# Performance work log

Measured on AMD Instinct MI355X. Metric: run time of the kernel, lower is better.

Reference implementation:

```python
import jax, jax.numpy as jnp
import numpy as np

N = 1_000_000
D_MODEL = 128
D_PRIN = 64        # d_principle: truncated projected dims used in traversal stage
R = 32             # nsw32 -> fixed out-degree
B = 128            # query batch
E = 32             # random32 entry points
EF = 64            # ef_search (beam width)
K = 10
N_ITERS = 8        # fixed number of beam-expansion rounds (jit-friendly traversal)


def setup_inputs() -> dict:
    key = jax.random.key(0)
    k1, k2, k3, k4, k5 = jax.random.split(key, 5)
    query = jax.random.normal(k1, (B, D_MODEL), jnp.float32)
    VT = jax.random.normal(k2, (D_MODEL, D_MODEL), jnp.float32) / jnp.sqrt(D_MODEL)
    storage = jax.random.normal(k3, (N, D_MODEL), jnp.float32)
    neighbors = jax.random.randint(k4, (N, R), 0, N, jnp.int32)
    entry_ids = jax.random.randint(k5, (E,), 0, N, jnp.int32)
    return {"query": query, "VT": VT, "storage": storage,
            "neighbors": neighbors, "entry_ids": entry_ids,
            "k": K, "ef_search": EF}


def _search(query, VT, storage, neighbors, entry_ids, k, ef_search):
    n = storage.shape[0]
    bq = query.shape[0]
    BIG = jnp.float32(1e30)

    # stage 0: project query into SVD basis; principle dims for traversal
    q_full = query @ VT.T                      # [B, d_model]
    q_p = q_full[:, :D_PRIN]                   # [B, d_p]
    storage_p = storage[:, :D_PRIN]            # [N, d_p]
    sq_p = jnp.sum(storage_p * storage_p, axis=-1)          # [N]
    qn = jnp.sum(q_p * q_p, axis=-1, keepdims=True)         # [B, 1]

    def dist_p(ids):  # squared L2 in principle dims, sentinel id >= n -> BIG
        c = jnp.clip(ids, 0, n - 1)
        d = sq_p[c] - 2.0 * jnp.einsum('bmd,bd->bm', storage_p[c], q_p) + qn
        return jnp.where(ids >= n, BIG, d)

    def dedup_topk(ids, dists, m):
        # sort by id, mask duplicate ids (same id -> same dist), keep best m
        order = jnp.argsort(ids, axis=-1)
        sid = jnp.take_along_axis(ids, order, axis=-1)
        sd = jnp.take_along_axis(dists, order, axis=-1)
        dup = jnp.concatenate(
            [jnp.zeros_like(sid[:, :1], dtype=bool), sid[:, 1:] == sid[:, :-1]], axis=-1)
        sd = jnp.where(dup | (sid >= n), BIG, sd)
        neg, idx = jax.lax.top_k(-sd, m)
        return jnp.take_along_axis(sid, idx, axis=-1), -neg

    # entry stage (random32): distances to fixed entry points
    ids0 = jnp.broadcast_to(entry_ids[None, :], (bq, entry_ids.shape[0]))
    d0 = dist_p(ids0)
    pad = ef_search - ids0.shape[1]
    beam_I = jnp.concatenate([ids0, jnp.full((bq, pad), n, dtype=ids0.dtype)], axis=-1)
    beam_D = jnp.concatenate([d0, jnp.full((bq, pad), BIG, dtype=d0.dtype)], axis=-1)
    beam_I, beam_D = dedup_topk(beam_I, beam_D, ef_search)

    # beam traversal over NSW neighbor lists (principle-dim distances)
    def step(carry, _):
        bI, bD = carry
        nbr = neighbors[jnp.clip(bI, 0, n - 1)]              # [B, ef, R]
        cand = jnp.where(bI[:, :, None] >= n, n, nbr).reshape(bq, -1)
        cD = dist_p(cand)
        aI = jnp.concatenate([bI, cand.astype(bI.dtype)], axis=-1)
        aD = jnp.concatenate([bD, cD], axis=-1)
        return dedup_topk(aI, aD, ef_search), None

    (beam_I, beam_D), _ = jax.lax.scan(step, (beam_I, beam_D), None, length=N_ITERS)

    # final stage: rerank beam with full-dimensional distances, return top-k
    vecs = storage[jnp.clip(beam_I, 0, n - 1)]               # [B, ef, d_model]
    diff = vecs - q_full[:, None, :]
    d_full = jnp.where(beam_I >= n, BIG, jnp.sum(diff * diff, axis=-1))
    neg, idx = jax.lax.top_k(-d_full, k)
    out_I = jnp.take_along_axis(beam_I, idx, axis=-1)
    return out_I, -neg


def reference(query, VT, storage, neighbors, entry_ids, k, ef_search):
    return _search(query, VT, storage, neighbors, entry_ids, k, ef_search)
```

## Files before the change

kernel.cpp:

```cpp
#include <hip/hip_runtime.h>

typedef unsigned long long ull;

#define N_PTS   1000000
#define DM      128
#define DP      64
#define RNB     32
#define ENT     32
#define EFS     64
#define KOUT    10
#define N_ITERS 8
#define NTH     1024
#define NWAVE   (NTH / 64)
#define HASHCAP 32768
#define MAXNEW  2048
#define BIGF    1e30f
#define PADKEY  0xFFFFFFFFFFFFFFFFull

__device__ __forceinline__ unsigned fkey_enc(float d) {
  unsigned b = __float_as_uint(d);
  return (b & 0x80000000u) ? ~b : (b | 0x80000000u);
}

__device__ __forceinline__ float dist_p(const float* __restrict__ storage,
                                        const float* qf, float qn, int id) {
  int c = id < 0 ? 0 : (id > N_PTS - 1 ? N_PTS - 1 : id);
  const float4* row = (const float4*)(storage + (size_t)c * DM);
  float sq = 0.f, dt = 0.f;
#pragma unroll
  for (int j = 0; j < DP / 4; ++j) {
    float4 s = row[j];
    sq = fmaf(s.x, s.x, sq); sq = fmaf(s.y, s.y, sq);
    sq = fmaf(s.z, s.z, sq); sq = fmaf(s.w, s.w, sq);
    dt = fmaf(s.x, qf[4*j+0], dt); dt = fmaf(s.y, qf[4*j+1], dt);
    dt = fmaf(s.z, qf[4*j+2], dt); dt = fmaf(s.w, qf[4*j+3], dt);
  }
  float d = sq - 2.f * dt + qn;
  return (id >= N_PTS) ? BIGF : d;
}

__device__ __forceinline__ bool visit_claim(int* htab, int id) {
  unsigned h = ((unsigned)id * 2654435761u) & (HASHCAP - 1);
  while (true) {
    int cur = htab[h];
    if (cur == id) return false;
    if (cur == -1) {
      int old = atomicCAS(&htab[h], -1, id);
      if (old == -1) return true;
      if (old == id) return false;
    }
    h = (h + 1) & (HASHCAP - 1);
  }
}

__device__ __forceinline__ ull wsort64(ull key, int lane) {
#pragma unroll
  for (int k = 2; k <= 64; k <<= 1) {
#pragma unroll
    for (int j = k >> 1; j > 0; j >>= 1) {
      ull other = __shfl_xor(key, j);
      bool up = ((lane & k) == 0);
      bool lower = ((lane & j) == 0);
      ull mn = key < other ? key : other;
      ull mx = key < other ? other : key;
      key = (up == lower) ? mn : mx;
    }
  }
  return key;
}

__device__ __forceinline__ ull wbmerge64(ull key, int lane) {
#pragma unroll
  for (int j = 32; j > 0; j >>= 1) {
    ull other = __shfl_xor(key, j);
    bool lower = ((lane & j) == 0);
    ull mn = key < other ? key : other;
    ull mx = key < other ? other : key;
    key = lower ? mn : mx;
  }
  return key;
}

__device__ __forceinline__ ull wmerge(ull a, ull b, int lane) {
  ull brev = __shfl_xor(b, 63);
  ull c = a < brev ? a : brev;
  return wbmerge64(c, lane);
}

__device__ __forceinline__ int wave_append(int* counter, bool want, int lane) {
  ull mask = __ballot(want);
  int pos = -1;
  if (mask) {
    int leader = __ffsll((long long)mask) - 1;
    int base = 0;
    if (lane == leader) base = atomicAdd(counter, (int)__popcll(mask));
    base = __shfl(base, leader);
    pos = base + (int)__popcll(mask & ((1ull << lane) - 1ull));
  }
  return pos;
}

__global__ __launch_bounds__(NTH) void search_kernel(
    const float* __restrict__ query,
    const float* __restrict__ VT,
    const float* __restrict__ storage,
    const int*   __restrict__ neighbors,
    const int*   __restrict__ entry_ids,
    float* __restrict__ out)
{
  __shared__ int   htab[HASHCAP];
  __shared__ ull   newkeys[MAXNEW];
  __shared__ ull   scratch[NWAVE * 64];
  __shared__ ull   beamkey[EFS];
  __shared__ int   beam_id[EFS];
  __shared__ float qf[DM];
  __shared__ float qloc[DM];
  __shared__ float qn_s;
  __shared__ int   nclaim, nc;
  __shared__ float dfull[EFS];

  int* evalids = (int*)scratch;

  const int b    = blockIdx.x;
  const int B    = gridDim.x;
  const int tid  = threadIdx.x;
  const int lane = tid & 63;
  const int wid  = tid >> 6;

  const ull FILLKEY = ((ull)fkey_enc(BIGF) << 32) | (unsigned)N_PTS;

  for (int i = tid; i < HASHCAP; i += NTH) htab[i] = -1;

  if (tid < DM) qloc[tid] = query[(size_t)b * DM + tid];
  __syncthreads();
  if (tid < DM) {
    const float* vrow = VT + (size_t)tid * DM;
    float acc = 0.f;
#pragma unroll 8
    for (int d = 0; d < DM; ++d) acc = fmaf(qloc[d], vrow[d], acc);
    qf[tid] = acc;
  }
  __syncthreads();
  if (tid == 0) {
    float acc = 0.f;
    for (int d = 0; d < DP; ++d) acc = fmaf(qf[d], qf[d], acc);
    qn_s = acc;
  }
  __syncthreads();
  const float qn = qn_s;

  if (wid == 0) {
    ull ek = PADKEY;
    if (lane < ENT) {
      int id = entry_ids[lane];
      if (visit_claim(htab, id)) {
        float d = dist_p(storage, qf, qn, id);
        ek = ((ull)fkey_enc(d) << 32) | (unsigned)id;
      }
    }
    ek = wsort64(ek, lane);
    if (ek == PADKEY) ek = FILLKEY;
    beamkey[lane] = ek;
    beam_id[lane] = (int)(ek & 0xFFFFFFFFull);
  }
  __syncthreads();

  for (int it = 0; it < N_ITERS; ++it) {
    ull kmax = beamkey[EFS - 1];
    if (tid == 0) { nclaim = 0; nc = 0; }
    __syncthreads();

#pragma unroll
    for (int ci = tid; ci < EFS * RNB; ci += NTH) {
      int e = ci >> 5;
      int r = ci & 31;
      int bid = beam_id[e];
      bool want = false;
      int cid = 0;
      if (bid < N_PTS) {
        cid = neighbors[(size_t)bid * RNB + r];
        want = visit_claim(htab, cid);
      }
      int pos = wave_append(&nclaim, want, lane);
      if (want) evalids[pos] = cid;
    }
    __syncthreads();

    int ne = nclaim;
    int ntrips = (ne + NTH - 1) / NTH;
    for (int t = 0; t < ntrips; ++t) {
      int i = t * NTH + tid;
      bool valid = i < ne;
      int cid = valid ? evalids[i] : 0;
      float d = dist_p(storage, qf, qn, cid);
      ull key = ((ull)fkey_enc(d) << 32) | (unsigned)cid;
      bool pass = valid && (key < kmax);
      int pos = wave_append(&nc, pass, lane);
      if (pass) newkeys[pos] = key;
    }
    __syncthreads();

    int cnt = nc;
    if (cnt == 0) break;

    ull tk = PADKEY;
    int nchunks = (cnt + 63) >> 6;
    for (int c = wid; c < nchunks; c += NWAVE) {
      int idx = (c << 6) + lane;
      ull v = (idx < cnt) ? newkeys[idx] : PADKEY;
      v = wsort64(v, lane);
      tk = wmerge(tk, v, lane);
    }
    __syncthreads();
    scratch[wid * 64 + lane] = tk;
    __syncthreads();

    ull m8 = PADKEY;
    if (wid < 8) {
      ull a  = scratch[(2 * wid) * 64 + lane];
      ull bb = scratch[(2 * wid + 1) * 64 + lane];
      m8 = wmerge(a, bb, lane);
    }
    __syncthreads();
    if (wid < 8) scratch[wid * 64 + lane] = m8;
    __syncthreads();
    if (wid == 0) {
      ull m0 = wmerge(scratch[0 * 64 + lane], scratch[1 * 64 + lane], lane);
      ull m1 = wmerge(scratch[2 * 64 + lane], scratch[3 * 64 + lane], lane);
      ull m2 = wmerge(scratch[4 * 64 + lane], scratch[5 * 64 + lane], lane);
      ull m3 = wmerge(scratch[6 * 64 + lane], scratch[7 * 64 + lane], lane);
      ull t0 = wmerge(m0, m1, lane);
      ull t1 = wmerge(m2, m3, lane);
      ull t2 = wmerge(t0, t1, lane);
      ull nb = wmerge(beamkey[lane], t2, lane);
      beamkey[lane] = nb;
      beam_id[lane] = (int)(nb & 0xFFFFFFFFull);
    }
    __syncthreads();
  }

  if (wid == 0) {
    int id = beam_id[lane];
    int c = id < 0 ? 0 : (id > N_PTS - 1 ? N_PTS - 1 : id);
    const float4* row = (const float4*)(storage + (size_t)c * DM);
    float acc = 0.f;
#pragma unroll
    for (int j = 0; j < DM / 4; ++j) {
      float4 s = row[j];
      float dx = s.x - qf[4*j+0]; acc = fmaf(dx, dx, acc);
      dx = s.y - qf[4*j+1]; acc = fmaf(dx, dx, acc);
      dx = s.z - qf[4*j+2]; acc = fmaf(dx, dx, acc);
      dx = s.w - qf[4*j+3]; acc = fmaf(dx, dx, acc);
    }
    float dv = (id >= N_PTS) ? BIGF : acc;
    dfull[lane] = dv;
    ull fk = ((ull)fkey_enc(dv) << 32) | (unsigned)lane;
    fk = wsort64(fk, lane);
    if (lane < KOUT) {
      int pos = (int)(fk & 0xFFFFFFFFull);
      out[(size_t)b * KOUT + lane] = (float)beam_id[pos];
      out[(size_t)B * KOUT + (size_t)b * KOUT + lane] = dfull[pos];
    }
  }
}

extern "C" void kernel_launch(void* const* d_in, const int* in_sizes, int n_in,
                              void* d_out, int out_size, void* d_ws, size_t ws_size,
                              hipStream_t stream) {
  const float* query     = (const float*)d_in[0];
  const float* VT        = (const float*)d_in[1];
  const float* storage   = (const float*)d_in[2];
  const int*   neighbors = (const int*)d_in[3];
  const int*   entry_ids = (const int*)d_in[4];
  float* out = (float*)d_out;

  int B = in_sizes[0] / DM;
  search_kernel<<<B, NTH, 0, stream>>>(query, VT, storage, neighbors, entry_ids, out);
}
```

Baseline: 130.2 us.

## Cooperative 16-lane distance evaluation with coalesced row loads and 512-thread blocks

Candidate distance computation now gives each 64-dim row to a group of 16 lanes that each load one float4 and reduce with shuffles. This replaces one thread per candidate walking its own row, so global loads become coalesced and four rows are kept in flight per wave. The block size drops from 1024 to 512 threads and the cross-wave merge tree is shortened to match, with scratch resized so merge outputs go to separate slots. The cost is shuffle-reduction overhead and only one lane in sixteen producing a key, plus fewer threads for the hash-claim phase.

```diff
diff --git a/kernel.cpp b/kernel.cpp
--- a/kernel.cpp
+++ b/kernel.cpp
@@ -9,11 +9,11 @@
 #define ENT     32
 #define EFS     64
 #define KOUT    10
-#define N_ITERS 8
-#define NTH     1024
+#define NITERS  8
+#define NTH     512
 #define NWAVE   (NTH / 64)
 #define HASHCAP 32768
-#define MAXNEW  2048
+#define MAXNEW  2112
 #define BIGF    1e30f
 #define PADKEY  0xFFFFFFFFFFFFFFFFull
 
@@ -110,10 +110,10 @@
 {
   __shared__ int   htab[HASHCAP];
   __shared__ ull   newkeys[MAXNEW];
-  __shared__ ull   scratch[NWAVE * 64];
+  __shared__ ull   scratch[1024];
   __shared__ ull   beamkey[EFS];
   __shared__ int   beam_id[EFS];
-  __shared__ float qf[DM];
+  __shared__ __align__(16) float qf[DM];
   __shared__ float qloc[DM];
   __shared__ float qn_s;
   __shared__ int   nclaim, nc;
@@ -126,6 +126,8 @@
   const int tid  = threadIdx.x;
   const int lane = tid & 63;
   const int wid  = tid >> 6;
+  const int grp  = lane >> 4;
+  const int sub  = lane & 15;
 
   const ull FILLKEY = ((ull)fkey_enc(BIGF) << 32) | (unsigned)N_PTS;
 
@@ -148,6 +150,8 @@
   }
   __syncthreads();
   const float qn = qn_s;
+
+  const float4 mq = ((const float4*)qf)[sub];
 
   if (wid == 0) {
     ull ek = PADKEY;
@@ -165,7 +169,7 @@
   }
   __syncthreads();
 
-  for (int it = 0; it < N_ITERS; ++it) {
+  for (int it = 0; it < NITERS; ++it) {
     ull kmax = beamkey[EFS - 1];
     if (tid == 0) { nclaim = 0; nc = 0; }
     __syncthreads();
@@ -187,16 +191,36 @@
     __syncthreads();
 
     int ne = nclaim;
-    int ntrips = (ne + NTH - 1) / NTH;
-    for (int t = 0; t < ntrips; ++t) {
-      int i = t * NTH + tid;
-      bool valid = i < ne;
-      int cid = valid ? evalids[i] : 0;
-      float d = dist_p(storage, qf, qn, cid);
-      ull key = ((ull)fkey_enc(d) << 32) | (unsigned)cid;
-      bool pass = valid && (key < kmax);
-      int pos = wave_append(&nc, pass, lane);
-      if (pass) newkeys[pos] = key;
+    for (int base = wid * 16; base < ne; base += NWAVE * 16) {
+      float4 s[4];
+      int cid[4];
+#pragma unroll
+      for (int u = 0; u < 4; ++u) {
+        int idx = base + u * 4 + grp;
+        cid[u] = (idx < ne) ? evalids[idx] : 0;
+        const float4* row = (const float4*)(storage + (size_t)cid[u] * DM);
+        s[u] = row[sub];
+      }
+#pragma unroll
+      for (int u = 0; u < 4; ++u) {
+        int idx = base + u * 4 + grp;
+        float4 v = s[u];
+        float psq = 0.f, pdt = 0.f;
+        psq = fmaf(v.x, v.x, psq); psq = fmaf(v.y, v.y, psq);
+        psq = fmaf(v.z, v.z, psq); psq = fmaf(v.w, v.w, psq);
+        pdt = fmaf(v.x, mq.x, pdt); pdt = fmaf(v.y, mq.y, pdt);
+        pdt = fmaf(v.z, mq.z, pdt); pdt = fmaf(v.w, mq.w, pdt);
+#pragma unroll
+        for (int j = 1; j < 16; j <<= 1) {
+          psq += __shfl_xor(psq, j);
+          pdt += __shfl_xor(pdt, j);
+        }
+        float d = psq - 2.f * pdt + qn;
+        ull key = ((ull)fkey_enc(d) << 32) | (unsigned)cid[u];
+        bool pass = (sub == 0) && (idx < ne) && (key < kmax);
+        int pos = wave_append(&nc, pass, lane);
+        if (pass) newkeys[pos] = key;
+      }
     }
     __syncthreads();
 
@@ -215,23 +239,16 @@
     scratch[wid * 64 + lane] = tk;
     __syncthreads();
 
-    ull m8 = PADKEY;
-    if (wid < 8) {
+    if (wid < 4) {
       ull a  = scratch[(2 * wid) * 64 + lane];
       ull bb = scratch[(2 * wid + 1) * 64 + lane];
-      m8 = wmerge(a, bb, lane);
-    }
-    __syncthreads();
-    if (wid < 8) scratch[wid * 64 + lane] = m8;
+      scratch[(NWAVE + wid) * 64 + lane] = wmerge(a, bb, lane);
+    }
     __syncthreads();
     if (wid == 0) {
-      ull m0 = wmerge(scratch[0 * 64 + lane], scratch[1 * 64 + lane], lane);
-      ull m1 = wmerge(scratch[2 * 64 + lane], scratch[3 * 64 + lane], lane);
-      ull m2 = wmerge(scratch[4 * 64 + lane], scratch[5 * 64 + lane], lane);
-      ull m3 = wmerge(scratch[6 * 64 + lane], scratch[7 * 64 + lane], lane);
-      ull t0 = wmerge(m0, m1, lane);
-      ull t1 = wmerge(m2, m3, lane);
-      ull t2 = wmerge(t0, t1, lane);
+      ull m0 = wmerge(scratch[(NWAVE + 0) * 64 + lane], scratch[(NWAVE + 1) * 64 + lane], lane);
+      ull m1 = wmerge(scratch[(NWAVE + 2) * 64 + lane], scratch[(NWAVE + 3) * 64 + lane], lane);
+      ull t2 = wmerge(m0, m1, lane);
       ull nb = wmerge(beamkey[lane], t2, lane);
       beamkey[lane] = nb;
       beam_id[lane] = (int)(nb & 0xFFFFFFFFull);
```

After: 146.7 us. +12.7%, slower.
